# Optimization experiments

Hardware: AMD Instinct MI355X
Metric: run time of the kernel (lower is better)

Reference implementation:

```python
import jax, jax.numpy as jnp
import numpy as np

# LinearAdderV1: out[b,o] = sum_i (input[b,i] + weight[o,i]); out *= bias[o]
# The broadcast-add-then-reduce is mathematically separable:
#   sum_i (x[b,i] + w[o,i]) = sum_i x[b,i] + sum_i w[o,i]
# so we compute it without materializing the (B, O, I) intermediate. Same math,
# identical up to fp summation order.

B = 4096
IN = 4096
OUT = 4096


def setup_inputs() -> dict:
    key = jax.random.key(0)
    k1, k2, k3 = jax.random.split(key, 3)
    inp = jax.random.normal(k1, (B, IN), dtype=jnp.float32)
    # kaiming_uniform-ish scale for weight, uniform bias in [-1/sqrt(fan_in), +)
    bound_w = float(np.sqrt(6.0 / ((1.0 + 5.0) * IN)))  # a=sqrt(5) => gain^2=2/(1+5)
    weight = jax.random.uniform(k2, (OUT, IN), dtype=jnp.float32, minval=-bound_w, maxval=bound_w)
    bound_b = float(1.0 / np.sqrt(IN))
    bias_param = jax.random.uniform(k3, (OUT,), dtype=jnp.float32, minval=-bound_b, maxval=bound_b)
    return {"input": inp, "weight": weight, "bias_param": bias_param}


def reference(input, weight, bias_param):
    # (B, 1) + (1, OUT) -> (B, OUT)
    x_sum = jnp.sum(input, axis=-1, keepdims=True)          # (B, 1)
    w_sum = jnp.sum(weight, axis=-1)                        # (OUT,)
    out = x_sum + w_sum[None, :]                            # (B, OUT)
    out = out * bias_param[None, :]
    return out
```

## Files before the change

### kernel.cpp

```cpp
#include <hip/hip_runtime.h>

#define B_DIM   4096
#define IN_DIM  4096
#define OUT_DIM 4096

typedef float floatx4 __attribute__((ext_vector_type(4)));

__global__ __launch_bounds__(256) void wsum_kernel(
    const float* __restrict__ weight, const float* __restrict__ bias,
    float* __restrict__ wb)
{
    const int wave = threadIdx.x >> 6;
    const int lane = threadIdx.x & 63;
    const int o    = blockIdx.x * 4 + wave;

    const floatx4* src4 = (const floatx4*)(weight + (size_t)o * IN_DIM);

    float s0 = 0.f, s1 = 0.f, s2 = 0.f, s3 = 0.f;
    #pragma unroll
    for (int k = 0; k < 16; k += 4) {
        floatx4 v0 = __builtin_nontemporal_load(&src4[lane + (k + 0) * 64]);
        floatx4 v1 = __builtin_nontemporal_load(&src4[lane + (k + 1) * 64]);
        floatx4 v2 = __builtin_nontemporal_load(&src4[lane + (k + 2) * 64]);
        floatx4 v3 = __builtin_nontemporal_load(&src4[lane + (k + 3) * 64]);
        s0 += (v0.x + v0.y) + (v0.z + v0.w);
        s1 += (v1.x + v1.y) + (v1.z + v1.w);
        s2 += (v2.x + v2.y) + (v2.z + v2.w);
        s3 += (v3.x + v3.y) + (v3.z + v3.w);
    }
    float s = (s0 + s1) + (s2 + s3);

    #pragma unroll
    for (int off = 32; off > 0; off >>= 1)
        s += __shfl_down(s, off, 64);

    if (lane == 0)
        wb[o] = s * bias[o];
}

__global__ __launch_bounds__(256) void fused_kernel(
    const float* __restrict__ input, const float* __restrict__ bias,
    const float* __restrict__ wb, float* __restrict__ out)
{
    const int b = blockIdx.x;
    const int t = threadIdx.x;

    const floatx4* in4 = (const floatx4*)(input + (size_t)b * IN_DIM);

    floatx4 v[4];
    #pragma unroll
    for (int k = 0; k < 4; ++k)
        v[k] = __builtin_nontemporal_load(&in4[t + k * 256]);

    float s = 0.f;
    #pragma unroll
    for (int k = 0; k < 4; ++k)
        s += (v[k].x + v[k].y) + (v[k].z + v[k].w);

    #pragma unroll
    for (int off = 32; off > 0; off >>= 1)
        s += __shfl_down(s, off, 64);

    __shared__ float sm[4];
    if ((t & 63) == 0) sm[t >> 6] = s;
    __syncthreads();
    const float xs = (sm[0] + sm[1]) + (sm[2] + sm[3]);

    const floatx4* bias4 = (const floatx4*)bias;
    const floatx4* wb4   = (const floatx4*)wb;
    floatx4* out4 = (floatx4*)out + (size_t)b * (OUT_DIM / 4);

    #pragma unroll
    for (int k = 0; k < 4; ++k) {
        const int i = t + k * 256;
        const floatx4 bi = bias4[i];
        const floatx4 w  = wb4[i];
        floatx4 r;
        r.x = fmaf(xs, bi.x, w.x);
        r.y = fmaf(xs, bi.y, w.y);
        r.z = fmaf(xs, bi.z, w.z);
        r.w = fmaf(xs, bi.w, w.w);
        __builtin_nontemporal_store(r, &out4[i]);
    }
}

extern "C" void kernel_launch(void* const* d_in, const int* in_sizes, int n_in,
                              void* d_out, int out_size, void* d_ws, size_t ws_size,
                              hipStream_t stream) {
    const float* input  = (const float*)d_in[0];
    const float* weight = (const float*)d_in[1];
    const float* bias   = (const float*)d_in[2];
    float* out = (float*)d_out;
    float* wb  = (float*)d_ws;

    wsum_kernel<<<OUT_DIM / 4, 256, 0, stream>>>(weight, bias, wb);
    fused_kernel<<<B_DIM, 256, 0, stream>>>(input, bias, wb, out);
}
```

Before: 163.6 us.

## Rebalance work: compute half the input row sums in the first kernel with LDS-direct loads

The first kernel now reduces both the weight rows and the first half of the input rows, using global_load_lds to stage data in LDS with a split waitcnt so it can sum one part while the rest is still loading. The second kernel launches half as many blocks. Each block writes two output rows: one uses a precomputed input sum, the other uses a row sum it reduces itself. This moves work out of the output-writing kernel, reuses the bias and weight-sum vectors across two rows, and raises the memory-level parallelism of the first kernel. In exchange, the first kernel becomes larger and uses 32KB of LDS per block, which may limit occupancy.

```diff
diff --git a/kernel.cpp b/kernel.cpp
--- a/kernel.cpp
+++ b/kernel.cpp
@@ -5,58 +5,97 @@
 #define OUT_DIM 4096
 
 typedef float floatx4 __attribute__((ext_vector_type(4)));
+typedef __attribute__((address_space(1))) const void global_void;
+typedef __attribute__((address_space(3))) void lds_void;
 
-__global__ __launch_bounds__(256) void wsum_kernel(
-    const float* __restrict__ weight, const float* __restrict__ bias,
-    float* __restrict__ wb)
+__global__ __launch_bounds__(256) void k1_stage_sums(
+    const float* __restrict__ input, const float* __restrict__ weight,
+    const float* __restrict__ bias, float* __restrict__ ws)
 {
+    __shared__ float4 buf[2048];
     const int wave = threadIdx.x >> 6;
     const int lane = threadIdx.x & 63;
-    const int o    = blockIdx.x * 4 + wave;
+    const int rid  = blockIdx.x * 4 + wave;
 
-    const floatx4* src4 = (const floatx4*)(weight + (size_t)o * IN_DIM);
+    const bool is_w = rid < 4096;
+    const float* src = is_w ? weight + (size_t)rid * IN_DIM
+                            : input  + (size_t)(rid - 4096) * IN_DIM;
+    const float4* g4 = (const float4*)src;
+    float4* lb = &buf[wave * 512];
 
-    float s0 = 0.f, s1 = 0.f, s2 = 0.f, s3 = 0.f;
+    float s = 0.f;
     #pragma unroll
-    for (int k = 0; k < 16; k += 4) {
-        floatx4 v0 = __builtin_nontemporal_load(&src4[lane + (k + 0) * 64]);
-        floatx4 v1 = __builtin_nontemporal_load(&src4[lane + (k + 1) * 64]);
-        floatx4 v2 = __builtin_nontemporal_load(&src4[lane + (k + 2) * 64]);
-        floatx4 v3 = __builtin_nontemporal_load(&src4[lane + (k + 3) * 64]);
-        s0 += (v0.x + v0.y) + (v0.z + v0.w);
-        s1 += (v1.x + v1.y) + (v1.z + v1.w);
-        s2 += (v2.x + v2.y) + (v2.z + v2.w);
-        s3 += (v3.x + v3.y) + (v3.z + v3.w);
+    for (int h = 0; h < 2; ++h) {
+        const float4* gh = g4 + h * 512;
+        #pragma unroll
+        for (int k = 0; k < 8; ++k)
+            __builtin_amdgcn_global_load_lds(
+                (global_void*)(gh + k * 64 + lane),
+                (lds_void*)(lb + k * 64), 16, 0, 0);
+
+        asm volatile("s_waitcnt vmcnt(4)" ::: "memory");
+        #pragma unroll
+        for (int k = 0; k < 4; ++k) {
+            float4 v = lb[k * 64 + lane];
+            s += (v.x + v.y) + (v.z + v.w);
+        }
+        asm volatile("s_waitcnt vmcnt(0)" ::: "memory");
+        #pragma unroll
+        for (int k = 4; k < 8; ++k) {
+            float4 v = lb[k * 64 + lane];
+            s += (v.x + v.y) + (v.z + v.w);
+        }
     }
-    float s = (s0 + s1) + (s2 + s3);
 
     #pragma unroll
     for (int off = 32; off > 0; off >>= 1)
         s += __shfl_down(s, off, 64);
 
-    if (lane == 0)
-        wb[o] = s * bias[o];
+    if (lane == 0) {
+        if (is_w) ws[4096 + rid] = s * bias[rid];
+        else      ws[rid - 4096] = s;
+    }
 }
 
-__global__ __launch_bounds__(256) void fused_kernel(
+__global__ __launch_bounds__(256) void k2_fused(
     const float* __restrict__ input, const float* __restrict__ bias,
-    const float* __restrict__ wb, float* __restrict__ out)
+    const float* __restrict__ ws, float* __restrict__ out)
 {
-    const int b = blockIdx.x;
+    const int i = blockIdx.x;
     const int t = threadIdx.x;
+    const int r = 2048 + i;
 
-    const floatx4* in4 = (const floatx4*)(input + (size_t)b * IN_DIM);
-
+    const floatx4* in4 = (const floatx4*)(input + (size_t)r * IN_DIM);
     floatx4 v[4];
     #pragma unroll
     for (int k = 0; k < 4; ++k)
         v[k] = __builtin_nontemporal_load(&in4[t + k * 256]);
 
+    const floatx4* bias4 = (const floatx4*)bias;
+    const floatx4* wb4   = (const floatx4*)(ws + 4096);
+    floatx4 bi[4], wv[4];
+    #pragma unroll
+    for (int k = 0; k < 4; ++k) {
+        bi[k] = bias4[t + k * 256];
+        wv[k] = wb4[t + k * 256];
+    }
+
+    const float xs_i = ws[i];
+    floatx4* oi = (floatx4*)out + (size_t)i * (OUT_DIM / 4);
+    #pragma unroll
+    for (int k = 0; k < 4; ++k) {
+        floatx4 rr;
+        rr.x = fmaf(xs_i, bi[k].x, wv[k].x);
+        rr.y = fmaf(xs_i, bi[k].y, wv[k].y);
+        rr.z = fmaf(xs_i, bi[k].z, wv[k].z);
+        rr.w = fmaf(xs_i, bi[k].w, wv[k].w);
+        __builtin_nontemporal_store(rr, &oi[t + k * 256]);
+    }
+
     float s = 0.f;
     #pragma unroll
     for (int k = 0; k < 4; ++k)
         s += (v[k].x + v[k].y) + (v[k].z + v[k].w);
-
     #pragma unroll
     for (int off = 32; off > 0; off >>= 1)
         s += __shfl_down(s, off, 64);
@@ -64,23 +103,17 @@
     __shared__ float sm[4];
     if ((t & 63) == 0) sm[t >> 6] = s;
     __syncthreads();
-    const float xs = (sm[0] + sm[1]) + (sm[2] + sm[3]);
+    const float xs_r = (sm[0] + sm[1]) + (sm[2] + sm[3]);
 
-    const floatx4* bias4 = (const floatx4*)bias;
-    const floatx4* wb4   = (const floatx4*)wb;
-    floatx4* out4 = (floatx4*)out + (size_t)b * (OUT_DIM / 4);
-
+    floatx4* orow = (floatx4*)out + (size_t)r * (OUT_DIM / 4);
     #pragma unroll
     for (int k = 0; k < 4; ++k) {
-        const int i = t + k * 256;
-        const floatx4 bi = bias4[i];
-        const floatx4 w  = wb4[i];
-        floatx4 r;
-        r.x = fmaf(xs, bi.x, w.x);
-        r.y = fmaf(xs, bi.y, w.y);
-        r.z = fmaf(xs, bi.z, w.z);
-        r.w = fmaf(xs, bi.w, w.w);
-        __builtin_nontemporal_store(r, &out4[i]);
+        floatx4 rr;
+        rr.x = fmaf(xs_r, bi[k].x, wv[k].x);
+        rr.y = fmaf(xs_r, bi[k].y, wv[k].y);
+        rr.z = fmaf(xs_r, bi[k].z, wv[k].z);
+        rr.w = fmaf(xs_r, bi[k].w, wv[k].w);
+        __builtin_nontemporal_store(rr, &orow[t + k * 256]);
     }
 }
 
@@ -91,8 +124,8 @@
     const float* weight = (const float*)d_in[1];
     const float* bias   = (const float*)d_in[2];
     float* out = (float*)d_out;
-    float* wb  = (float*)d_ws;
+    float* ws  = (float*)d_ws;
 
-    wsum_kernel<<<OUT_DIM / 4, 256, 0, stream>>>(weight, bias, wb);
-    fused_kernel<<<B_DIM, 256, 0, stream>>>(input, bias, wb, out);
+    k1_stage_sums<<<(4096 + 2048) / 4, 256, 0, stream>>>(input, weight, bias, ws);
+    k2_fused<<<2048, 256, 0, stream>>>(input, bias, ws, out);
 }
```

Measured after the change: 170.1 us. +3.9%, slower.

## Split row reductions into a partial-sum kernel, combine kernel, and epilogue

Applied to the files above, without the earlier changes.

Both the input and the weight row sums now come from one partials kernel. Each wave handles half-rows of both tensors, with two half-rows in flight at a time, and writes per-lane partial sums to workspace. A combine kernel reduces the partials into xs and wb, and the epilogue becomes a pure streaming write. The aim is to raise memory-level parallelism for the read-heavy reduction and take the reduction off the write-bound epilogue. The cost is an extra launch and a 4 MB round trip for the partials, and the nontemporal loads are dropped.

```diff
diff --git a/kernel.cpp b/kernel.cpp
--- a/kernel.cpp
+++ b/kernel.cpp
@@ -6,65 +6,78 @@
 
 typedef float floatx4 __attribute__((ext_vector_type(4)));
 
-__global__ __launch_bounds__(256) void wsum_kernel(
-    const float* __restrict__ weight, const float* __restrict__ bias,
-    float* __restrict__ wb)
+#define PART_FLOATS (16384 * 64)
+
+__device__ __forceinline__ float sum8(const floatx4* v) {
+    float s0 = 0.f, s1 = 0.f, s2 = 0.f, s3 = 0.f;
+    s0 = (v[0].x + v[0].y) + (v[0].z + v[0].w);
+    s1 = (v[1].x + v[1].y) + (v[1].z + v[1].w);
+    s2 = (v[2].x + v[2].y) + (v[2].z + v[2].w);
+    s3 = (v[3].x + v[3].y) + (v[3].z + v[3].w);
+    s0 += (v[4].x + v[4].y) + (v[4].z + v[4].w);
+    s1 += (v[5].x + v[5].y) + (v[5].z + v[5].w);
+    s2 += (v[6].x + v[6].y) + (v[6].z + v[6].w);
+    s3 += (v[7].x + v[7].y) + (v[7].z + v[7].w);
+    return (s0 + s1) + (s2 + s3);
+}
+
+__global__ __launch_bounds__(256, 4) void k1a_partials(
+    const float* __restrict__ input, const float* __restrict__ weight,
+    float* __restrict__ part)
 {
     const int wave = threadIdx.x >> 6;
     const int lane = threadIdx.x & 63;
-    const int o    = blockIdx.x * 4 + wave;
+    const int wg   = blockIdx.x * 4 + wave;
 
-    const floatx4* src4 = (const floatx4*)(weight + (size_t)o * IN_DIM);
+    const floatx4* b0 = (const floatx4*)(input  + (size_t)wg * 2048);
+    const floatx4* b1 = (const floatx4*)(input  + (size_t)(wg + 4096) * 2048);
+    const floatx4* b2 = (const floatx4*)(weight + (size_t)wg * 2048);
+    const floatx4* b3 = (const floatx4*)(weight + (size_t)(wg + 4096) * 2048);
 
-    float s0 = 0.f, s1 = 0.f, s2 = 0.f, s3 = 0.f;
+    floatx4 a[8], b[8];
     #pragma unroll
-    for (int k = 0; k < 16; k += 4) {
-        floatx4 v0 = __builtin_nontemporal_load(&src4[lane + (k + 0) * 64]);
-        floatx4 v1 = __builtin_nontemporal_load(&src4[lane + (k + 1) * 64]);
-        floatx4 v2 = __builtin_nontemporal_load(&src4[lane + (k + 2) * 64]);
-        floatx4 v3 = __builtin_nontemporal_load(&src4[lane + (k + 3) * 64]);
-        s0 += (v0.x + v0.y) + (v0.z + v0.w);
-        s1 += (v1.x + v1.y) + (v1.z + v1.w);
-        s2 += (v2.x + v2.y) + (v2.z + v2.w);
-        s3 += (v3.x + v3.y) + (v3.z + v3.w);
-    }
-    float s = (s0 + s1) + (s2 + s3);
+    for (int k = 0; k < 8; ++k) a[k] = b0[lane + k * 64];
+    #pragma unroll
+    for (int k = 0; k < 8; ++k) b[k] = b1[lane + k * 64];
 
+    part[(size_t)wg * 64 + lane] = sum8(a);
+    #pragma unroll
+    for (int k = 0; k < 8; ++k) a[k] = b2[lane + k * 64];
+
+    part[(size_t)(wg + 4096) * 64 + lane] = sum8(b);
+    #pragma unroll
+    for (int k = 0; k < 8; ++k) b[k] = b3[lane + k * 64];
+
+    part[(size_t)(wg + 8192) * 64 + lane] = sum8(a);
+    part[(size_t)(wg + 12288) * 64 + lane] = sum8(b);
+}
+
+__global__ __launch_bounds__(256) void k1b_combine(
+    const float* __restrict__ part, const float* __restrict__ bias,
+    float* __restrict__ xs, float* __restrict__ wb)
+{
+    const int wave = threadIdx.x >> 6;
+    const int lane = threadIdx.x & 63;
+    const int row  = blockIdx.x * 4 + wave;
+
+    float s = part[(size_t)row * 128 + lane] + part[(size_t)row * 128 + 64 + lane];
     #pragma unroll
     for (int off = 32; off > 0; off >>= 1)
         s += __shfl_down(s, off, 64);
 
-    if (lane == 0)
-        wb[o] = s * bias[o];
+    if (lane == 0) {
+        if (row < B_DIM) xs[row] = s;
+        else             wb[row - B_DIM] = s * bias[row - B_DIM];
+    }
 }
 
-__global__ __launch_bounds__(256) void fused_kernel(
-    const float* __restrict__ input, const float* __restrict__ bias,
+__global__ __launch_bounds__(256) void k2_epilogue(
+    const float* __restrict__ bias, const float* __restrict__ xs,
     const float* __restrict__ wb, float* __restrict__ out)
 {
     const int b = blockIdx.x;
     const int t = threadIdx.x;
-
-    const floatx4* in4 = (const floatx4*)(input + (size_t)b * IN_DIM);
-
-    floatx4 v[4];
-    #pragma unroll
-    for (int k = 0; k < 4; ++k)
-        v[k] = __builtin_nontemporal_load(&in4[t + k * 256]);
-
-    float s = 0.f;
-    #pragma unroll
-    for (int k = 0; k < 4; ++k)
-        s += (v[k].x + v[k].y) + (v[k].z + v[k].w);
-
-    #pragma unroll
-    for (int off = 32; off > 0; off >>= 1)
-        s += __shfl_down(s, off, 64);
-
-    __shared__ float sm[4];
-    if ((t & 63) == 0) sm[t >> 6] = s;
-    __syncthreads();
-    const float xs = (sm[0] + sm[1]) + (sm[2] + sm[3]);
+    const float xsb = xs[b];
 
     const floatx4* bias4 = (const floatx4*)bias;
     const floatx4* wb4   = (const floatx4*)wb;
@@ -76,10 +89,10 @@
         const floatx4 bi = bias4[i];
         const floatx4 w  = wb4[i];
         floatx4 r;
-        r.x = fmaf(xs, bi.x, w.x);
-        r.y = fmaf(xs, bi.y, w.y);
-        r.z = fmaf(xs, bi.z, w.z);
-        r.w = fmaf(xs, bi.w, w.w);
+        r.x = fmaf(xsb, bi.x, w.x);
+        r.y = fmaf(xsb, bi.y, w.y);
+        r.z = fmaf(xsb, bi.z, w.z);
+        r.w = fmaf(xsb, bi.w, w.w);
         __builtin_nontemporal_store(r, &out4[i]);
     }
 }
@@ -90,9 +103,12 @@
     const float* input  = (const float*)d_in[0];
     const float* weight = (const float*)d_in[1];
     const float* bias   = (const float*)d_in[2];
-    float* out = (float*)d_out;
-    float* wb  = (float*)d_ws;
+    float* out  = (float*)d_out;
+    float* part = (float*)d_ws;
+    float* xs   = part + PART_FLOATS;
+    float* wb   = xs + B_DIM;
 
-    wsum_kernel<<<OUT_DIM / 4, 256, 0, stream>>>(weight, bias, wb);
-    fused_kernel<<<B_DIM, 256, 0, stream>>>(input, bias, wb, out);
+    k1a_partials<<<1024, 256, 0, stream>>>(input, weight, part);
+    k1b_combine<<<2048, 256, 0, stream>>>(part, bias, xs, wb);
+    k2_epilogue<<<B_DIM, 256, 0, stream>>>(bias, xs, wb, out);
 }
```

Measured after the change: 173.1 us. 1.06x slower.
